# Kernel tuning notes

Measured on AMD Instinct MI355X. Metric: run time of the kernel, lower is better.

Reference implementation:

```python
import jax, jax.numpy as jnp
import numpy as np

D_MODEL = 768
N_HEADS = 12
HEAD_DIM = D_MODEL // N_HEADS


def setup_inputs() -> dict:
    key = jax.random.key(0)
    ks = jax.random.split(key, 9)
    s = 1.0 / np.sqrt(D_MODEL)
    return {
        "x": jax.random.normal(ks[0], (2, 2048, D_MODEL), dtype=jnp.float32),
        "Wq": jax.random.uniform(ks[1], (D_MODEL, D_MODEL), minval=-s, maxval=s, dtype=jnp.float32),
        "bq": jax.random.uniform(ks[2], (D_MODEL,), minval=-s, maxval=s, dtype=jnp.float32),
        "Wk": jax.random.uniform(ks[3], (D_MODEL, D_MODEL), minval=-s, maxval=s, dtype=jnp.float32),
        "bk": jax.random.uniform(ks[4], (D_MODEL,), minval=-s, maxval=s, dtype=jnp.float32),
        "Wv": jax.random.uniform(ks[5], (D_MODEL, D_MODEL), minval=-s, maxval=s, dtype=jnp.float32),
        "bv": jax.random.uniform(ks[6], (D_MODEL,), minval=-s, maxval=s, dtype=jnp.float32),
        "Wo": jax.random.uniform(ks[7], (D_MODEL, D_MODEL), minval=-s, maxval=s, dtype=jnp.float32),
        "bo": jax.random.uniform(ks[8], (D_MODEL,), minval=-s, maxval=s, dtype=jnp.float32),
    }


def reference(x, Wq, bq, Wk, bk, Wv, bv, Wo, bo):
    B, S, D = x.shape
    H, Hd = N_HEADS, HEAD_DIM
    # nn.Linear: y = x @ W.T + b
    q = (x @ Wq.T + bq).reshape(B, S, H, Hd).transpose(0, 2, 1, 3)  # [B,H,S,Hd]
    k = (x @ Wk.T + bk).reshape(B, S, H, Hd).transpose(0, 2, 1, 3)
    v = (x @ Wv.T + bv).reshape(B, S, H, Hd).transpose(0, 2, 1, 3)
    scores = jnp.einsum('bhqd,bhkd->bhqk', q, k) / np.sqrt(Hd)  # [B,H,S,S]
    attn = jax.nn.softmax(scores, axis=-1)
    out = jnp.einsum('bhqk,bhkd->bhqd', attn, v)  # [B,H,S,Hd]
    out = out.transpose(0, 2, 1, 3).reshape(B, S, D)
    return out @ Wo.T + bo
```

## Files before the change

kernel.cpp:

```cpp
#include <hip/hip_runtime.h>

#define D_MODEL 768
#define SEQ 2048
#define BATCH 2
#define NHEADS 12
#define HDIM 64
#define M_TOTAL (BATCH*SEQ)
#define NQK (2*D_MODEL)

typedef __attribute__((ext_vector_type(8))) short short8;
typedef __attribute__((ext_vector_type(4))) float floatx4;

static __device__ __forceinline__ unsigned short f2bf(float f) {
    union { float f; unsigned int u; } v; v.f = f;
    unsigned int r = (v.u + 0x7fffu + ((v.u >> 16) & 1u)) >> 16;
    return (unsigned short)r;
}

static __device__ __forceinline__ void async16(void* lds, const void* g) {
    __builtin_amdgcn_global_load_lds(
        (const __attribute__((address_space(1))) unsigned int*)g,
        (__attribute__((address_space(3))) unsigned int*)lds, 16, 0, 0);
}

#define X8    393216
#define W8    73728
__global__ __launch_bounds__(256) void cvt_all_kernel(
    const float* __restrict__ x,  const float* __restrict__ Wq,
    const float* __restrict__ Wk, const float* __restrict__ Wv,
    const float* __restrict__ Wo,
    unsigned short* __restrict__ xb, unsigned short* __restrict__ wqk,
    unsigned short* __restrict__ wvb, unsigned short* __restrict__ wob)
{
    int i = blockIdx.x * 256 + threadIdx.x;
    const float* src; unsigned short* dst;
    if (i < X8)                { src = x  + (size_t)i*8;            dst = xb  + (size_t)i*8; }
    else if (i < X8 + W8)      { int j = i - X8;                    src = Wq + (size_t)j*8; dst = wqk + (size_t)j*8; }
    else if (i < X8 + 2*W8)    { int j = i - (X8 + W8);             src = Wk + (size_t)j*8; dst = wqk + 589824 + (size_t)j*8; }
    else if (i < X8 + 3*W8)    { int j = i - (X8 + 2*W8);           src = Wv + (size_t)j*8; dst = wvb + (size_t)j*8; }
    else                       { int j = i - (X8 + 3*W8);           src = Wo + (size_t)j*8; dst = wob + (size_t)j*8; }
    const float4* s = (const float4*)src;
    float4 a = s[0], b = s[1];
    short8 o;
    o[0]=(short)f2bf(a.x); o[1]=(short)f2bf(a.y); o[2]=(short)f2bf(a.z); o[3]=(short)f2bf(a.w);
    o[4]=(short)f2bf(b.x); o[5]=(short)f2bf(b.y); o[6]=(short)f2bf(b.z); o[7]=(short)f2bf(b.w);
    *(short8*)dst = o;
}

__global__ __launch_bounds__(256) void bias_qk_kernel(
    const float* __restrict__ bq, const float* __restrict__ bk, float* __restrict__ dst)
{
    int i = blockIdx.x * 256 + threadIdx.x;
    if (i < 768) dst[i] = bq[i];
    else dst[i] = bk[i - 768];
}

template<int MI>
__device__ __forceinline__ void gemm_core(
    const unsigned short* __restrict__ A, const unsigned short* __restrict__ W,
    int m0, int n0, unsigned short* smem, floatx4 (&acc)[MI][4], int t)
{
    char* AsB = (char*)smem;
    char* WsB = (char*)(smem + MI*32*64);
    const int lane = t & 63;
    const int quad = lane >> 4, l = lane & 15;
    const int wvv = t >> 6, wr = wvv >> 1, wc = wvv & 1;
    const int base_off = t & ~63;

    for (int kt = 0; kt < 12; ++kt) {
        __syncthreads();
#pragma unroll
        for (int it = 0; it < MI; ++it) {
            int slot = it*256 + t;
            int r = slot >> 3, cpos = slot & 7, c = cpos ^ (r & 7);
            async16(AsB + (size_t)(it*256 + base_off)*16, A + (size_t)(m0 + r)*768 + kt*64 + c*8);
        }
#pragma unroll
        for (int it = 0; it < 4; ++it) {
            int slot = it*256 + t;
            int r = slot >> 3, cpos = slot & 7, c = cpos ^ (r & 7);
            async16(WsB + (size_t)(it*256 + base_off)*16, W + (size_t)(n0 + r)*768 + kt*64 + c*8);
        }
        __syncthreads();
#pragma unroll
        for (int ks = 0; ks < 2; ++ks) {
            short8 af[MI], wf[4];
#pragma unroll
            for (int mi = 0; mi < MI; ++mi) {
                int m = wr*(MI*16) + mi*16 + l;
                af[mi] = *(const short8*)(AsB + m*128 + (((ks*4+quad) ^ (m&7))*16));
            }
#pragma unroll
            for (int ni = 0; ni < 4; ++ni) {
                int n = wc*64 + ni*16 + l;
                wf[ni] = *(const short8*)(WsB + n*128 + (((ks*4+quad) ^ (n&7))*16));
            }
#pragma unroll
            for (int mi = 0; mi < MI; ++mi)
#pragma unroll
                for (int ni = 0; ni < 4; ++ni)
                    acc[mi][ni] = __builtin_amdgcn_mfma_f32_16x16x32_bf16(
                        af[mi], wf[ni], acc[mi][ni], 0, 0, 0);
        }
    }
}

__global__ __launch_bounds__(256) void gemm_qkvt_kernel(
    const unsigned short* __restrict__ xb, const unsigned short* __restrict__ wqk,
    const unsigned short* __restrict__ wvb,
    const float* __restrict__ bqk, const float* __restrict__ bv,
    unsigned short* __restrict__ qkout, unsigned short* __restrict__ vtout)
{
    __shared__ unsigned short smem[256*64];
    const int t = threadIdx.x;
    int bid = blockIdx.x;
    const bool isqk = bid < 384;
    const unsigned short *A, *W; int m0, n0;
    if (isqk) { A = xb;  W = wqk; m0 = (bid/12)*128; n0 = (bid%12)*128; }
    else { int v = bid - 384; A = wvb; W = xb; m0 = (v%6)*128; n0 = (v/6)*128; }

    floatx4 acc[4][4];
#pragma unroll
    for (int i=0;i<4;i++)
#pragma unroll
        for (int j=0;j<4;j++) acc[i][j] = (floatx4){0.f,0.f,0.f,0.f};

    gemm_core<4>(A, W, m0, n0, smem, acc, t);

    const int lane = t & 63, quad = lane >> 4, l = lane & 15;
    const int wvv = t >> 6, wr = wvv >> 1, wc = wvv & 1;

    __syncthreads();
#pragma unroll
    for (int mi=0;mi<4;mi++)
#pragma unroll
        for (int ni=0;ni<4;ni++) {
            int col = wc*64 + ni*16 + l;
            float bcol = isqk ? bqk[n0 + col] : 0.f;
#pragma unroll
            for (int r=0;r<4;r++) {
                int row = wr*64 + mi*16 + quad*4 + r;
                float bb = isqk ? bcol : bv[m0 + row];
                smem[row*128 + col] = f2bf(acc[mi][ni][r] + bb);
            }
        }
    __syncthreads();
#pragma unroll
    for (int i=0;i<8;i++) {
        int slot = i*256 + t;
        int r = slot >> 4, c = slot & 15;
        short8 val = *(const short8*)(smem + r*128 + c*8);
        if (isqk) {
            *(short8*)(qkout + (size_t)(m0+r)*NQK + n0 + c*8) = val;
        } else {
            int f = m0 + r, tok = n0 + c*8;
            *(short8*)(vtout + ((size_t)(tok>>11)*768 + f)*SEQ + (tok & (SEQ-1))) = val;
        }
    }
}

__global__ __launch_bounds__(256) void gemm_out_kernel(
    const unsigned short* __restrict__ ab, const unsigned short* __restrict__ wob,
    const float* __restrict__ bo, float* __restrict__ out)
{
    __shared__ unsigned short smem[192*64];
    const int t = threadIdx.x;
    int bid = blockIdx.x;
    int m0 = (bid/6)*64, n0 = (bid%6)*128;

    floatx4 acc[2][4];
#pragma unroll
    for (int i=0;i<2;i++)
#pragma unroll
        for (int j=0;j<4;j++) acc[i][j] = (floatx4){0.f,0.f,0.f,0.f};

    gemm_core<2>(ab, wob, m0, n0, smem, acc, t);

    const int lane = t & 63, quad = lane >> 4, l = lane & 15;
    const int wvv = t >> 6, wr = wvv >> 1, wc = wvv & 1;
#pragma unroll
    for (int mi=0;mi<2;mi++)
#pragma unroll
        for (int ni=0;ni<4;ni++) {
            int col = n0 + wc*64 + ni*16 + l;
            float bb = bo[col];
#pragma unroll
            for (int r=0;r<4;r++) {
                int row = m0 + wr*32 + mi*16 + quad*4 + r;
                out[(size_t)row*768 + col] = acc[mi][ni][r] + bb;
            }
        }
}

__global__ __launch_bounds__(256) void attn_kernel(
    const unsigned short* __restrict__ qk,
    const unsigned short* __restrict__ vt,
    unsigned short* __restrict__ aout)
{
    __shared__ unsigned short Ks[128*64];
    __shared__ unsigned short Vs[64*128];
    __shared__ unsigned short Ps[64*128];
    char* KsB = (char*)Ks; char* VsB = (char*)Vs; char* PsB = (char*)Ps;

    const int t = threadIdx.x, lane = t & 63, wvv = t >> 6;
    const int quad = lane >> 4, l = lane & 15;
    const int q0 = blockIdx.x * 64;
    const int h = blockIdx.y, b = blockIdx.z;
    const size_t rowbase = (size_t)b * SEQ;
    const int base_off = t & ~63;

    short8 qf[2];
    {
        const unsigned short* g = qk + (rowbase + q0 + wvv*16 + l)*NQK + h*64 + quad*8;
        qf[0] = *(const short8*)g;
        qf[1] = *(const short8*)(g + 32);
    }

    floatx4 oacc[4];
#pragma unroll
    for (int i=0;i<4;i++) oacc[i] = (floatx4){0.f,0.f,0.f,0.f};
    float lpart[4] = {0.f, 0.f, 0.f, 0.f};

    for (int kt = 0; kt < SEQ/128; ++kt) {
        __syncthreads();
#pragma unroll
        for (int it=0; it<4; ++it) {
            int slot = it*256 + t;
            int r = slot >> 3, cpos = slot & 7, c = cpos ^ (r & 7);
            const unsigned short* g = qk + (rowbase + kt*128 + r)*NQK + 768 + h*64 + c*8;
            async16(KsB + (size_t)(it*256 + base_off)*16, g);
        }
#pragma unroll
        for (int it=0; it<4; ++it) {
            int slot = it*256 + t;
            int r = slot >> 4, cpos = slot & 15, c = cpos ^ (r & 15);
            const unsigned short* g = vt + ((size_t)b*768 + h*64 + r)*SEQ + kt*128 + c*8;
            async16(VsB + (size_t)(it*256 + base_off)*16, g);
        }
        __syncthreads();

        floatx4 sacc[8];
#pragma unroll
        for (int i=0;i<8;i++) sacc[i] = (floatx4){0.f,0.f,0.f,0.f};
#pragma unroll
        for (int ks=0; ks<2; ++ks)
#pragma unroll
            for (int ni=0; ni<8; ++ni) {
                int n = ni*16 + l;
                short8 kf = *(const short8*)(KsB + n*128 + (((ks*4+quad) ^ (n&7))*16));
                sacc[ni] = __builtin_amdgcn_mfma_f32_16x16x32_bf16(qf[ks], kf, sacc[ni], 0, 0, 0);
            }

#pragma unroll
        for (int r=0; r<4; ++r) {
            int row = wvv*16 + quad*4 + r;
            float psum = 0.f;
#pragma unroll
            for (int ni=0; ni<8; ++ni) {
                float p = __expf(sacc[ni][r]*0.125f - 3.0f);
                psum += p;
                int cc = (ni*16 + l) >> 3;
                int pos = cc ^ (row & 15);
                Ps[row*128 + pos*8 + (l & 7)] = f2bf(p);
            }
            lpart[r] += psum;
        }

#pragma unroll
        for (int kk=0; kk<4; ++kk) {
            int m = wvv*16 + l;
            short8 pf = *(const short8*)(PsB + m*256 + (((kk*4+quad) ^ (m&15))*16));
#pragma unroll
            for (int ni=0; ni<4; ++ni) {
                int n = ni*16 + l;
                short8 vf = *(const short8*)(VsB + n*256 + (((kk*4+quad) ^ (n&15))*16));
                oacc[ni] = __builtin_amdgcn_mfma_f32_16x16x32_bf16(pf, vf, oacc[ni], 0, 0, 0);
            }
        }
    }

    float lrow[4];
#pragma unroll
    for (int r=0;r<4;r++) {
        float lr = lpart[r];
        lr += __shfl_xor(lr, 1);
        lr += __shfl_xor(lr, 2);
        lr += __shfl_xor(lr, 4);
        lr += __shfl_xor(lr, 8);
        lrow[r] = lr;
    }

    __syncthreads();
#pragma unroll
    for (int r=0;r<4;r++) {
        float inv = 1.0f / lrow[r];
        int row = wvv*16 + quad*4 + r;
#pragma unroll
        for (int ni=0;ni<4;ni++)
            Ps[row*64 + ni*16 + l] = f2bf(oacc[ni][r] * inv);
    }
    __syncthreads();
#pragma unroll
    for (int it=0; it<2; ++it) {
        int slot = it*256 + t;
        int r = slot >> 3, c = slot & 7;
        *(short8*)(aout + (rowbase + q0 + r)*768 + h*64 + c*8) = *(const short8*)(Ps + r*64 + c*8);
    }
}

extern "C" void kernel_launch(void* const* d_in, const int* in_sizes, int n_in,
                              void* d_out, int out_size, void* d_ws, size_t ws_size,
                              hipStream_t stream)
{
    const float* x  = (const float*)d_in[0];
    const float* Wq = (const float*)d_in[1];
    const float* bq = (const float*)d_in[2];
    const float* Wk = (const float*)d_in[3];
    const float* bk = (const float*)d_in[4];
    const float* Wv = (const float*)d_in[5];
    const float* bv = (const float*)d_in[6];
    const float* Wo = (const float*)d_in[7];
    const float* bo = (const float*)d_in[8];

    unsigned short* ws = (unsigned short*)d_ws;
    unsigned short* xb  = ws;
    unsigned short* wqk = xb  + (size_t)3145728;
    unsigned short* wvb = wqk + (size_t)1179648;
    unsigned short* wob = wvb + (size_t)589824;
    unsigned short* qkb = wob + (size_t)589824;
    unsigned short* vtb = qkb + (size_t)6291456;
    unsigned short* ab  = vtb + (size_t)3145728;
    float* bqk = (float*)(ab + (size_t)3145728);

    cvt_all_kernel<<<(X8 + 4*W8)/256, 256, 0, stream>>>(x, Wq, Wk, Wv, Wo, xb, wqk, wvb, wob);
    bias_qk_kernel<<<6, 256, 0, stream>>>(bq, bk, bqk);

    gemm_qkvt_kernel<<<576, 256, 0, stream>>>(xb, wqk, wvb, bqk, bv, qkb, vtb);

    attn_kernel<<<dim3(SEQ/64, NHEADS, BATCH), 256, 0, stream>>>(qkb, vtb, ab);

    gemm_out_kernel<<<384, 256, 0, stream>>>(ab, wob, bo, (float*)d_out);
}
```

Measured before the change: 204.1 us.

## Double-buffer GEMM and attention tiles, keep P in registers, fuse bias copy

Both GEMMs and the attention kernel now double-buffer their LDS tiles, so the next K-slice is loaded asynchronously while the current one is computed. The attention kernel is rebuilt around 128 threads per block, with each wave owning 32 query rows. It computes S transposed so the bf16 P fragments stay in registers and feed 16x16x16 MFMAs directly, removing the P round-trip through LDS, and it uses exp2 with a folded scale. The separate bias-copy kernel is merged into the conversion kernel to save a launch. The cost is doubled LDS use per block and a different occupancy profile for attention. Softmax still relies on a fixed offset of -3 rather than a running max, as before.

Measured after the change: 217.4 us. 1.07x slower.

```diff
diff --git a/kernel.cpp b/kernel.cpp
--- a/kernel.cpp
+++ b/kernel.cpp
@@ -9,7 +9,11 @@
 #define NQK (2*D_MODEL)
 
 typedef __attribute__((ext_vector_type(8))) short short8;
+typedef __attribute__((ext_vector_type(4))) short short4_t;
 typedef __attribute__((ext_vector_type(4))) float floatx4;
+
+#define MFMA_PV(a,b,c) __builtin_amdgcn_mfma_f32_16x16x16bf16_1k(a,b,c,0,0,0)
+#define EXP2(x) __builtin_amdgcn_exp2f(x)
 
 static __device__ __forceinline__ unsigned short f2bf(float f) {
     union { float f; unsigned int u; } v; v.f = f;
@@ -25,20 +29,29 @@
 
 #define X8    393216
 #define W8    73728
+#define CVT_N (X8 + 4*W8)
+#define CVT_BLOCKS (CVT_N/256 + 6)
 __global__ __launch_bounds__(256) void cvt_all_kernel(
     const float* __restrict__ x,  const float* __restrict__ Wq,
     const float* __restrict__ Wk, const float* __restrict__ Wv,
-    const float* __restrict__ Wo,
+    const float* __restrict__ Wo, const float* __restrict__ bq,
+    const float* __restrict__ bk,
     unsigned short* __restrict__ xb, unsigned short* __restrict__ wqk,
-    unsigned short* __restrict__ wvb, unsigned short* __restrict__ wob)
+    unsigned short* __restrict__ wvb, unsigned short* __restrict__ wob,
+    float* __restrict__ bqk)
 {
     int i = blockIdx.x * 256 + threadIdx.x;
+    if (i >= CVT_N) {
+        int j = i - CVT_N;
+        if (j < 1536) bqk[j] = (j < 768) ? bq[j] : bk[j - 768];
+        return;
+    }
     const float* src; unsigned short* dst;
-    if (i < X8)                { src = x  + (size_t)i*8;            dst = xb  + (size_t)i*8; }
-    else if (i < X8 + W8)      { int j = i - X8;                    src = Wq + (size_t)j*8; dst = wqk + (size_t)j*8; }
-    else if (i < X8 + 2*W8)    { int j = i - (X8 + W8);             src = Wk + (size_t)j*8; dst = wqk + 589824 + (size_t)j*8; }
-    else if (i < X8 + 3*W8)    { int j = i - (X8 + 2*W8);           src = Wv + (size_t)j*8; dst = wvb + (size_t)j*8; }
-    else                       { int j = i - (X8 + 3*W8);           src = Wo + (size_t)j*8; dst = wob + (size_t)j*8; }
+    if (i < X8)             { src = x  + (size_t)i*8;            dst = xb  + (size_t)i*8; }
+    else if (i < X8 + W8)   { int j = i - X8;          src = Wq + (size_t)j*8; dst = wqk + (size_t)j*8; }
+    else if (i < X8 + 2*W8) { int j = i - (X8 + W8);   src = Wk + (size_t)j*8; dst = wqk + 589824 + (size_t)j*8; }
+    else if (i < X8 + 3*W8) { int j = i - (X8 + 2*W8); src = Wv + (size_t)j*8; dst = wvb + (size_t)j*8; }
+    else                    { int j = i - (X8 + 3*W8); src = Wo + (size_t)j*8; dst = wob + (size_t)j*8; }
     const float4* s = (const float4*)src;
     float4 a = s[0], b = s[1];
     short8 o;
@@ -47,41 +60,40 @@
     *(short8*)dst = o;
 }
 
-__global__ __launch_bounds__(256) void bias_qk_kernel(
-    const float* __restrict__ bq, const float* __restrict__ bk, float* __restrict__ dst)
-{
-    int i = blockIdx.x * 256 + threadIdx.x;
-    if (i < 768) dst[i] = bq[i];
-    else dst[i] = bk[i - 768];
-}
-
 template<int MI>
-__device__ __forceinline__ void gemm_core(
+__device__ __forceinline__ void gemm_core_db(
     const unsigned short* __restrict__ A, const unsigned short* __restrict__ W,
     int m0, int n0, unsigned short* smem, floatx4 (&acc)[MI][4], int t)
 {
-    char* AsB = (char*)smem;
-    char* WsB = (char*)(smem + MI*32*64);
-    const int lane = t & 63;
-    const int quad = lane >> 4, l = lane & 15;
+    const int ASZ = MI*32*64;
+    const int BSZ = ASZ + 8192;
+    const int quad = (t >> 4) & 3, l = t & 15;
     const int wvv = t >> 6, wr = wvv >> 1, wc = wvv & 1;
     const int base_off = t & ~63;
 
+    auto stage = [&](int buf, int kt) {
+        char* AsB = (char*)(smem + buf*BSZ);
+        char* WsB = (char*)(smem + buf*BSZ + ASZ);
+#pragma unroll
+        for (int it = 0; it < MI; ++it) {
+            int slot = it*256 + t;
+            int r = slot >> 3, c = (slot & 7) ^ (r & 7);
+            async16(AsB + (size_t)(it*256 + base_off)*16, A + (size_t)(m0+r)*768 + kt*64 + c*8);
+        }
+#pragma unroll
+        for (int it = 0; it < 4; ++it) {
+            int slot = it*256 + t;
+            int r = slot >> 3, c = (slot & 7) ^ (r & 7);
+            async16(WsB + (size_t)(it*256 + base_off)*16, W + (size_t)(n0+r)*768 + kt*64 + c*8);
+        }
+    };
+
+    stage(0, 0);
     for (int kt = 0; kt < 12; ++kt) {
         __syncthreads();
-#pragma unroll
-        for (int it = 0; it < MI; ++it) {
-            int slot = it*256 + t;
-            int r = slot >> 3, cpos = slot & 7, c = cpos ^ (r & 7);
-            async16(AsB + (size_t)(it*256 + base_off)*16, A + (size_t)(m0 + r)*768 + kt*64 + c*8);
-        }
-#pragma unroll
-        for (int it = 0; it < 4; ++it) {
-            int slot = it*256 + t;
-            int r = slot >> 3, cpos = slot & 7, c = cpos ^ (r & 7);
-            async16(WsB + (size_t)(it*256 + base_off)*16, W + (size_t)(n0 + r)*768 + kt*64 + c*8);
-        }
-        __syncthreads();
+        if (kt < 11) stage((kt+1)&1, kt+1);
+        const char* AsB = (const char*)(smem + (kt&1)*BSZ);
+        const char* WsB = (const char*)(smem + (kt&1)*BSZ + ASZ);
 #pragma unroll
         for (int ks = 0; ks < 2; ++ks) {
             short8 af[MI], wf[4];
@@ -111,7 +123,7 @@
     const float* __restrict__ bqk, const float* __restrict__ bv,
     unsigned short* __restrict__ qkout, unsigned short* __restrict__ vtout)
 {
-    __shared__ unsigned short smem[256*64];
+    __shared__ unsigned short smem[2*16384];
     const int t = threadIdx.x;
     int bid = blockIdx.x;
     const bool isqk = bid < 384;
@@ -125,7 +137,7 @@
 #pragma unroll
         for (int j=0;j<4;j++) acc[i][j] = (floatx4){0.f,0.f,0.f,0.f};
 
-    gemm_core<4>(A, W, m0, n0, smem, acc, t);
+    gemm_core_db<4>(A, W, m0, n0, smem, acc, t);
 
     const int lane = t & 63, quad = lane >> 4, l = lane & 15;
     const int wvv = t >> 6, wr = wvv >> 1, wc = wvv & 1;
@@ -163,7 +175,7 @@
     const unsigned short* __restrict__ ab, const unsigned short* __restrict__ wob,
     const float* __restrict__ bo, float* __restrict__ out)
 {
-    __shared__ unsigned short smem[192*64];
+    __shared__ unsigned short smem[2*12288];
     const int t = threadIdx.x;
     int bid = blockIdx.x;
     int m0 = (bid/6)*64, n0 = (bid%6)*128;
@@ -174,7 +186,7 @@
 #pragma unroll
         for (int j=0;j<4;j++) acc[i][j] = (floatx4){0.f,0.f,0.f,0.f};
 
-    gemm_core<2>(ab, wob, m0, n0, smem, acc, t);
+    gemm_core_db<2>(ab, wob, m0, n0, smem, acc, t);
 
     const int lane = t & 63, quad = lane >> 4, l = lane & 15;
     const int wvv = t >> 6, wr = wvv >> 1, wc = wvv & 1;
@@ -192,119 +204,135 @@
         }
 }
 
-__global__ __launch_bounds__(256) void attn_kernel(
+__global__ __launch_bounds__(128) void attn_kernel(
     const unsigned short* __restrict__ qk,
     const unsigned short* __restrict__ vt,
     unsigned short* __restrict__ aout)
 {
-    __shared__ unsigned short Ks[128*64];
-    __shared__ unsigned short Vs[64*128];
-    __shared__ unsigned short Ps[64*128];
-    char* KsB = (char*)Ks; char* VsB = (char*)Vs; char* PsB = (char*)Ps;
-
-    const int t = threadIdx.x, lane = t & 63, wvv = t >> 6;
-    const int quad = lane >> 4, l = lane & 15;
+    __shared__ unsigned short Ks[2][128*64];
+    __shared__ unsigned short Vs[2][64*128];
+    const int t = threadIdx.x;
+    const int lane = t & 63, w = t >> 6;
+    const int l16 = lane & 15, quad = lane >> 4;
     const int q0 = blockIdx.x * 64;
     const int h = blockIdx.y, b = blockIdx.z;
     const size_t rowbase = (size_t)b * SEQ;
+    const size_t vbase = ((size_t)(b*NHEADS + h))*HDIM*SEQ;
     const int base_off = t & ~63;
 
-    short8 qf[2];
-    {
-        const unsigned short* g = qk + (rowbase + q0 + wvv*16 + l)*NQK + h*64 + quad*8;
-        qf[0] = *(const short8*)g;
-        qf[1] = *(const short8*)(g + 32);
-    }
-
-    floatx4 oacc[4];
-#pragma unroll
-    for (int i=0;i<4;i++) oacc[i] = (floatx4){0.f,0.f,0.f,0.f};
-    float lpart[4] = {0.f, 0.f, 0.f, 0.f};
+    short8 qf[2][2];
+#pragma unroll
+    for (int qt = 0; qt < 2; ++qt) {
+        const unsigned short* qr = qk + (rowbase + q0 + w*32 + qt*16 + l16)*NQK + h*64;
+        qf[qt][0] = *(const short8*)(qr + quad*8);
+        qf[qt][1] = *(const short8*)(qr + 32 + quad*8);
+    }
+
+    auto stageK = [&](int buf, int kt) {
+        char* dst = (char*)Ks[buf];
+#pragma unroll
+        for (int it = 0; it < 8; ++it) {
+            int slot = it*128 + t;
+            int r = slot >> 3, c = (slot & 7) ^ (r & 7);
+            async16(dst + (size_t)(it*128 + base_off)*16,
+                    qk + (rowbase + kt*128 + r)*NQK + 768 + h*64 + c*8);
+        }
+    };
+    auto stageV = [&](int buf, int kt) {
+        char* dst = (char*)Vs[buf];
+#pragma unroll
+        for (int it = 0; it < 8; ++it) {
+            int slot = it*128 + t;
+            int d = slot >> 4, c = (slot & 15) ^ (d & 15);
+            async16(dst + (size_t)(it*128 + base_off)*16,
+                    vt + vbase + (size_t)d*SEQ + kt*128 + c*8);
+        }
+    };
+
+    floatx4 oacc[2][4];
+#pragma unroll
+    for (int qt=0;qt<2;qt++)
+#pragma unroll
+        for (int i=0;i<4;i++) oacc[qt][i] = (floatx4){0.f,0.f,0.f,0.f};
+    float lsum[2] = {0.f, 0.f};
+    short4_t pf[2][8];
+
+    stageK(0, 0); stageV(0, 0);
+
+    const float C1 = 0.18033688011112042f;
+    const float C2 = -4.32808512266689f;
 
     for (int kt = 0; kt < SEQ/128; ++kt) {
         __syncthreads();
-#pragma unroll
-        for (int it=0; it<4; ++it) {
-            int slot = it*256 + t;
-            int r = slot >> 3, cpos = slot & 7, c = cpos ^ (r & 7);
-            const unsigned short* g = qk + (rowbase + kt*128 + r)*NQK + 768 + h*64 + c*8;
-            async16(KsB + (size_t)(it*256 + base_off)*16, g);
-        }
-#pragma unroll
-        for (int it=0; it<4; ++it) {
-            int slot = it*256 + t;
-            int r = slot >> 4, cpos = slot & 15, c = cpos ^ (r & 15);
-            const unsigned short* g = vt + ((size_t)b*768 + h*64 + r)*SEQ + kt*128 + c*8;
-            async16(VsB + (size_t)(it*256 + base_off)*16, g);
-        }
-        __syncthreads();
-
-        floatx4 sacc[8];
-#pragma unroll
-        for (int i=0;i<8;i++) sacc[i] = (floatx4){0.f,0.f,0.f,0.f};
-#pragma unroll
-        for (int ks=0; ks<2; ++ks)
-#pragma unroll
-            for (int ni=0; ni<8; ++ni) {
-                int n = ni*16 + l;
-                short8 kf = *(const short8*)(KsB + n*128 + (((ks*4+quad) ^ (n&7))*16));
-                sacc[ni] = __builtin_amdgcn_mfma_f32_16x16x32_bf16(qf[ks], kf, sacc[ni], 0, 0, 0);
-            }
-
-#pragma unroll
-        for (int r=0; r<4; ++r) {
-            int row = wvv*16 + quad*4 + r;
-            float psum = 0.f;
-#pragma unroll
-            for (int ni=0; ni<8; ++ni) {
-                float p = __expf(sacc[ni][r]*0.125f - 3.0f);
-                psum += p;
-                int cc = (ni*16 + l) >> 3;
-                int pos = cc ^ (row & 15);
-                Ps[row*128 + pos*8 + (l & 7)] = f2bf(p);
-            }
-            lpart[r] += psum;
-        }
-
-#pragma unroll
-        for (int kk=0; kk<4; ++kk) {
-            int m = wvv*16 + l;
-            short8 pf = *(const short8*)(PsB + m*256 + (((kk*4+quad) ^ (m&15))*16));
-#pragma unroll
-            for (int ni=0; ni<4; ++ni) {
-                int n = ni*16 + l;
-                short8 vf = *(const short8*)(VsB + n*256 + (((kk*4+quad) ^ (n&15))*16));
-                oacc[ni] = __builtin_amdgcn_mfma_f32_16x16x32_bf16(pf, vf, oacc[ni], 0, 0, 0);
-            }
-        }
-    }
-
-    float lrow[4];
-#pragma unroll
-    for (int r=0;r<4;r++) {
-        float lr = lpart[r];
-        lr += __shfl_xor(lr, 1);
-        lr += __shfl_xor(lr, 2);
-        lr += __shfl_xor(lr, 4);
-        lr += __shfl_xor(lr, 8);
-        lrow[r] = lr;
-    }
-
+        if (kt < SEQ/128 - 1) { stageK((kt+1)&1, kt+1); stageV((kt+1)&1, kt+1); }
+        const char* KsB = (const char*)Ks[kt&1];
+        const char* VsB = (const char*)Vs[kt&1];
+
+#pragma unroll
+        for (int mt = 0; mt < 8; ++mt) {
+            int key = mt*16 + l16;
+            short8 kf0 = *(const short8*)(KsB + key*128 + ((quad     ^ (l16&7))*16));
+            short8 kf1 = *(const short8*)(KsB + key*128 + (((4+quad) ^ (l16&7))*16));
+#pragma unroll
+            for (int qt = 0; qt < 2; ++qt) {
+                floatx4 s = (floatx4){0.f,0.f,0.f,0.f};
+                s = __builtin_amdgcn_mfma_f32_16x16x32_bf16(kf0, qf[qt][0], s, 0, 0, 0);
+                s = __builtin_amdgcn_mfma_f32_16x16x32_bf16(kf1, qf[qt][1], s, 0, 0, 0);
+                float p0 = EXP2(fmaf(s[0], C1, C2));
+                float p1 = EXP2(fmaf(s[1], C1, C2));
+                float p2 = EXP2(fmaf(s[2], C1, C2));
+                float p3 = EXP2(fmaf(s[3], C1, C2));
+                lsum[qt] += (p0 + p1) + (p2 + p3);
+                short4_t pk;
+                pk[0] = (short)f2bf(p0); pk[1] = (short)f2bf(p1);
+                pk[2] = (short)f2bf(p2); pk[3] = (short)f2bf(p3);
+                pf[qt][mt] = pk;
+            }
+        }
+
+#pragma unroll
+        for (int mt = 0; mt < 8; ++mt) {
+#pragma unroll
+            for (int ni = 0; ni < 4; ++ni) {
+                int row = ni*16 + l16;
+                short4_t vf = *(const short4_t*)(VsB + row*256 +
+                                (((2*mt + (quad>>1)) ^ l16) & 15)*16 + (quad&1)*8);
+                oacc[0][ni] = MFMA_PV(pf[0][mt], vf, oacc[0][ni]);
+                oacc[1][ni] = MFMA_PV(pf[1][mt], vf, oacc[1][ni]);
+            }
+        }
+    }
+
+#pragma unroll
+    for (int qt = 0; qt < 2; ++qt) {
+        float v = lsum[qt];
+        v += __shfl_xor(v, 16);
+        v += __shfl_xor(v, 32);
+        lsum[qt] = v;
+    }
+    float inv[2][4];
+#pragma unroll
+    for (int qt = 0; qt < 2; ++qt)
+#pragma unroll
+        for (int r = 0; r < 4; ++r)
+            inv[qt][r] = 1.0f / __shfl(lsum[qt], quad*4 + r);
+
+    unsigned short* Ob = Ks[0];
+#pragma unroll
+    for (int qt = 0; qt < 2; ++qt)
+#pragma unroll
+        for (int ni = 0; ni < 4; ++ni)
+#pragma unroll
+            for (int r = 0; r < 4; ++r) {
+                int row = w*32 + qt*16 + quad*4 + r;
+                Ob[row*72 + ni*16 + l16] = f2bf(oacc[qt][ni][r] * inv[qt][r]);
+            }
     __syncthreads();
 #pragma unroll
-    for (int r=0;r<4;r++) {
-        float inv = 1.0f / lrow[r];
-        int row = wvv*16 + quad*4 + r;
-#pragma unroll
-        for (int ni=0;ni<4;ni++)
-            Ps[row*64 + ni*16 + l] = f2bf(oacc[ni][r] * inv);
-    }
-    __syncthreads();
-#pragma unroll
-    for (int it=0; it<2; ++it) {
-        int slot = it*256 + t;
+    for (int it = 0; it < 4; ++it) {
+        int slot = it*128 + t;
         int r = slot >> 3, c = slot & 7;
-        *(short8*)(aout + (rowbase + q0 + r)*768 + h*64 + c*8) = *(const short8*)(Ps + r*64 + c*8);
+        *(short8*)(aout + (rowbase + q0 + r)*768 + h*64 + c*8) = *(const short8*)(Ob + r*72 + c*8);
     }
 }
 
@@ -332,12 +360,12 @@
     unsigned short* ab  = vtb + (size_t)3145728;
     float* bqk = (float*)(ab + (size_t)3145728);
 
-    cvt_all_kernel<<<(X8 + 4*W8)/256, 256, 0, stream>>>(x, Wq, Wk, Wv, Wo, xb, wqk, wvb, wob);
-    bias_qk_kernel<<<6, 256, 0, stream>>>(bq, bk, bqk);
+    cvt_all_kernel<<<CVT_BLOCKS, 256, 0, stream>>>(x, Wq, Wk, Wv, Wo, bq, bk,
+                                                   xb, wqk, wvb, wob, bqk);
 
     gemm_qkvt_kernel<<<576, 256, 0, stream>>>(xb, wqk, wvb, bqk, bv, qkb, vtb);
 
-    attn_kernel<<<dim3(SEQ/64, NHEADS, BATCH), 256, 0, stream>>>(qkb, vtb, ab);
+    attn_kernel<<<dim3(SEQ/64, NHEADS, BATCH), 128, 0, stream>>>(qkb, vtb, ab);
 
     gemm_out_kernel<<<384, 256, 0, stream>>>(ab, wob, bo, (float*)d_out);
 }
```
